# Performance work log

Hardware: AMD Instinct MI355X
Metric: run time of the kernel (lower is better)

Reference implementation:

```python
import jax, jax.numpy as jnp
import numpy as np

B, N = 4, 512
C_IN, H, W = 1024, 48, 48
IMG_H, IMG_W = 48.0, 48.0
CNN_EMB, BOX_EMB, GCN_OUT = 512, 256, 512
ROWS, COLS = 58, 30
ALPHA = 5.0
K_EDGES = 8 * N  # edges kept per image per graph

# all directed pairs (i != j) of a fully-connected graph on N nodes
_ii, _jj = np.meshgrid(np.arange(N), np.arange(N), indexing='ij')
_m = _ii != _jj
PAIRS = jnp.asarray(np.stack([_ii[_m], _jj[_m]], axis=1).astype(np.int32))  # [E,2]


def setup_inputs():
    key = jax.random.key(0)
    ks = jax.random.split(key, 12)
    x = jax.random.normal(ks[0], (B, C_IN, H, W), jnp.float32)
    # valid boxes (x1<x2, y1<y2) inside the 48x48 feature map
    p = jax.random.uniform(ks[1], (B, N, 2, 2), minval=0.0, maxval=float(W) - 2.0)
    lo = jnp.min(p, axis=2)
    hi = jnp.max(p, axis=2) + 1.0
    boxes = jnp.concatenate([lo, hi], axis=-1)  # [B,N,4] x1,y1,x2,y2

    def lin(k, fi, fo):
        return jax.random.normal(k, (fi, fo), jnp.float32) / np.sqrt(fi)

    return {
        'input': x, 'boxes': boxes,
        'im_scales': jnp.ones((B,), jnp.float32),
        'pdls': jnp.zeros((B,), jnp.float32),
        'pdts': jnp.zeros((B,), jnp.float32),
        'W_dec': jax.random.normal(ks[2], (256, C_IN, 3, 3), jnp.float32) / np.sqrt(C_IN * 9.0),
        'b_dec': jnp.zeros((256,), jnp.float32),
        'W_box': lin(ks[3], 4, BOX_EMB), 'b_box': jnp.zeros((BOX_EMB,), jnp.float32),
        'W_cnn': lin(ks[4], 256 * 4, CNN_EMB), 'b_cnn': jnp.zeros((CNN_EMB,), jnp.float32),
        'W_grow': lin(ks[5], CNN_EMB + BOX_EMB, GCN_OUT), 'b_grow': jnp.zeros((GCN_OUT,), jnp.float32),
        'W_gcol': lin(ks[6], CNN_EMB + BOX_EMB, GCN_OUT), 'b_gcol': jnp.zeros((GCN_OUT,), jnp.float32),
        'W_rcls': lin(ks[7], GCN_OUT, 2 * (ROWS - 1) * 2), 'b_rcls': jnp.zeros((2 * (ROWS - 1) * 2,), jnp.float32),
        'W_ccls': lin(ks[8], GCN_OUT, 2 * (COLS - 1) * 2), 'b_ccls': jnp.zeros((2 * (COLS - 1) * 2,), jnp.float32),
    }


def _bilinear(feat, bidx, py, px):
    # feat [B,C,H,W]; py,px [M,4] sample coords -> [M,4,C]
    Hh, Ww = feat.shape[2], feat.shape[3]
    py = jnp.clip(py, 0.0, Hh - 1.0)
    px = jnp.clip(px, 0.0, Ww - 1.0)
    y0 = jnp.floor(py).astype(jnp.int32)
    x0 = jnp.floor(px).astype(jnp.int32)
    y1 = jnp.minimum(y0 + 1, Hh - 1)
    x1 = jnp.minimum(x0 + 1, Ww - 1)
    wy = (py - y0)[..., None]
    wx = (px - x0)[..., None]
    b = bidx[:, None]
    f00 = feat[b, :, y0, x0]
    f01 = feat[b, :, y0, x1]
    f10 = feat[b, :, y1, x0]
    f11 = feat[b, :, y1, x1]
    return f00 * (1 - wy) * (1 - wx) + f01 * (1 - wy) * wx + f10 * wy * (1 - wx) + f11 * wy * wx


def _roi_align_2x2(feat, boxes, bidx):
    # roi_align output_size=2, spatial_scale=1, one sample per bin (bin center)
    x1, y1, x2, y2 = boxes[:, 0], boxes[:, 1], boxes[:, 2], boxes[:, 3]
    bw = (x2 - x1) / 2.0
    bh = (y2 - y1) / 2.0
    offs = jnp.array([0.5, 1.5], jnp.float32)
    sx = x1[:, None] + offs * bw[:, None]  # [M,2]
    sy = y1[:, None] + offs * bh[:, None]
    py = sy[:, jnp.array([0, 0, 1, 1])]  # (iy, ix) ordering
    px = sx[:, jnp.array([0, 1, 0, 1])]
    val = _bilinear(feat, bidx, py, px)  # [M,4,C]
    return jnp.transpose(val, (0, 2, 1)).reshape(val.shape[0], -1)  # [M, C*2*2]


def _edge_attrs(boxes_i, scale, pdl, pdt):
    org = (boxes_i - jnp.stack([pdl, pdt, pdl, pdt])) / scale
    cx = (org[:, 0] + org[:, 2]) * 0.5
    cy = (org[:, 1] + org[:, 3]) * 0.5
    tb_w = jnp.max(org[:, jnp.array([0, 2])])
    tb_h = jnp.max(org[:, jnp.array([1, 3])])
    s, d = PAIRS[:, 0], PAIRS[:, 1]
    row_attr = jnp.exp(-jnp.square((cy[s] - cy[d]) * ALPHA / tb_h))
    col_attr = jnp.exp(-jnp.square((cx[s] - cx[d]) * ALPHA / tb_w))
    rv, ri = jax.lax.top_k(row_attr, K_EDGES)
    cv, ci = jax.lax.top_k(col_attr, K_EDGES)
    return rv, PAIRS[ri], cv, PAIRS[ci]


def _gcn(x, Wg, bg, edges, ew, num_nodes):
    # PyG GCNConv: self-loops with weight 1, symmetric normalization
    loop = jnp.arange(num_nodes, dtype=edges.dtype)
    src = jnp.concatenate([edges[0], loop])
    dst = jnp.concatenate([edges[1], loop])
    w = jnp.concatenate([ew, jnp.ones((num_nodes,), ew.dtype)])
    deg = jax.ops.segment_sum(w, dst, num_segments=num_nodes)
    dis = jax.lax.rsqrt(deg)  # deg >= 1 thanks to self-loops
    norm = dis[src] * w * dis[dst]
    xw = x @ Wg
    agg = jax.ops.segment_sum(norm[:, None] * xw[src], dst, num_segments=num_nodes)
    return agg + bg


def _forward(input, boxes, im_scales, pdls, pdts, W_dec, b_dec, W_box, b_box,
             W_cnn, b_cnn, W_grow, b_grow, W_gcol, b_gcol, W_rcls, b_rcls, W_ccls, b_ccls):
    Bn = B * N
    flat = boxes.reshape(Bn, 4)
    # box features (relative center / size)
    cx = (flat[:, 0] + flat[:, 2]) / 2.0
    cy = (flat[:, 1] + flat[:, 3]) / 2.0
    bf = jnp.stack([cx / IMG_W, cy / IMG_H,
                    (flat[:, 2] - flat[:, 0]) / IMG_W,
                    (flat[:, 3] - flat[:, 1]) / IMG_H], axis=1)
    box_feat = jax.nn.relu(bf @ W_box + b_box)
    # decode conv + relu
    dec = jax.lax.conv_general_dilated(input, W_dec, (1, 1), 'SAME',
                                       dimension_numbers=('NCHW', 'OIHW', 'NCHW'))
    dec = jax.nn.relu(dec + b_dec[None, :, None, None])
    # roi-align 2x2 + cnn embedding
    bidx = jnp.repeat(jnp.arange(B, dtype=jnp.int32), N)
    cnn = _roi_align_2x2(dec, flat, bidx)
    cnn_feat = jax.nn.relu(cnn @ W_cnn + b_cnn)
    # per-image dense graph -> top-8N row/col edges
    rv, re, cv, ce = jax.vmap(_edge_attrs)(boxes, im_scales, pdls, pdts)
    off = (jnp.arange(B, dtype=jnp.int32) * N)[:, None, None]
    row_edge = (re + off).reshape(-1, 2).T  # [2, B*K]
    col_edge = (ce + off).reshape(-1, 2).T
    row_w = rv.reshape(-1)
    col_w = cv.reshape(-1)
    fusion = jnp.concatenate([box_feat, cnn_feat], axis=1)  # [Bn, 768]
    row_feat = jax.nn.relu(_gcn(fusion, W_grow, b_grow, row_edge, row_w, Bn))
    col_feat = jax.nn.relu(_gcn(fusion, W_gcol, b_gcol, col_edge, col_w, Bn))
    row_score = jax.nn.leaky_relu(row_feat @ W_rcls + b_rcls, 0.01).reshape(Bn, 2, ROWS - 1, 2)
    col_score = jax.nn.leaky_relu(col_feat @ W_ccls + b_ccls, 0.01).reshape(Bn, 2, COLS - 1, 2)
    return row_score, col_score


def reference(input, boxes, im_scales, pdls, pdts, W_dec, b_dec, W_box, b_box,
              W_cnn, b_cnn, W_grow, b_grow, W_gcol, b_gcol, W_rcls, b_rcls, W_ccls, b_ccls):
    return _forward(input, boxes, im_scales, pdls, pdts, W_dec, b_dec, W_box, b_box,
                    W_cnn, b_cnn, W_grow, b_grow, W_gcol, b_gcol,
                    W_rcls, b_rcls, W_ccls, b_ccls)
```

## Files before the change

kernel.cpp:

```cpp
#include <hip/hip_runtime.h>
#include <cstdint>
#include <math.h>

typedef unsigned int u32;
typedef unsigned long long u64;
typedef unsigned short ushort;

typedef __attribute__((ext_vector_type(8))) _Float16 f16x8;
typedef __attribute__((ext_vector_type(4))) _Float16 f16x4;
typedef __attribute__((ext_vector_type(4))) float f32x4;

#define NB    4
#define BnN   2048
#define NE    261632
#define NCHUNK 16
#define ECHUNK 16352
#define KEDGE 4096
#define TIECAP 2048
#define PSLICE 2359296
#define MS    64
#define TS    64

#define GLD16(gsrc, ldst)                                                    \
    __builtin_amdgcn_global_load_lds(                                        \
        (const __attribute__((address_space(1))) void*)(gsrc),               \
        (__attribute__((address_space(3))) void*)(ldst), 16, 0, 0)

__global__ __launch_bounds__(256) void cvt_x_kernel(
    const float* __restrict__ in, _Float16* __restrict__ xf)
{
    __shared__ _Float16 sh[64][49];
    int cg = blockIdx.x, y = blockIdx.y, b = blockIdx.z;
    int tid = threadIdx.x;
    for (int i = tid; i < 64 * 48; i += 256) {
        int cl = i / 48, x = i - cl * 48;
        sh[cl][x] = (_Float16)in[(((size_t)b * 1024 + cg * 64 + cl) * 48 + y) * 48 + x];
    }
    __syncthreads();
    for (int i = tid; i < 64 * 48; i += 256) {
        int x = i / 64, cl = i - x * 64;
        xf[((size_t)(b * 48 + y) * 48 + x) * 1024 + cg * 64 + cl] = sh[cl][x];
    }
}

__global__ __launch_bounds__(256) void cvt_w_kernel(
    const float* __restrict__ W, _Float16* __restrict__ wf)
{
    __shared__ _Float16 sh[9216];
    int o = blockIdx.x, tid = threadIdx.x;
    for (int g = tid; g < 9216; g += 256)
        sh[g] = (_Float16)W[(size_t)o * 9216 + g];
    __syncthreads();
    for (int g = tid; g < 9216; g += 256) {
        int tap = g >> 10, ch = g & 1023;
        wf[(size_t)o * 9216 + g] = sh[ch * 9 + tap];
    }
}

__global__ __launch_bounds__(256) void cvt_t5_kernel(
    const float* __restrict__ Wc,  _Float16* __restrict__ WcT,
    const float* __restrict__ Wgr, _Float16* __restrict__ WgrT,
    const float* __restrict__ Wgc, _Float16* __restrict__ WgcT,
    const float* __restrict__ Wr,  _Float16* __restrict__ WrT,
    const float* __restrict__ Wcc, _Float16* __restrict__ WccT)
{
    __shared__ _Float16 sh[32][33];
    int bid = blockIdx.x;
    const float* in; _Float16* out; int K, N, tx0, ty0, ntx;
    if (bid < 512)       { in = Wc;  out = WcT;  K = 1024; N = 512; ntx = 16; bid -= 0;    }
    else if (bid < 896)  { in = Wgr; out = WgrT; K = 768;  N = 512; ntx = 16; bid -= 512;  }
    else if (bid < 1280) { in = Wgc; out = WgcT; K = 768;  N = 512; ntx = 16; bid -= 896;  }
    else if (bid < 1408) { in = Wr;  out = WrT;  K = 512;  N = 228; ntx = 8;  bid -= 1280; }
    else                 { in = Wcc; out = WccT; K = 512;  N = 116; ntx = 4;  bid -= 1408; }
    tx0 = (bid % ntx) * 32;
    ty0 = (bid / ntx) * 32;
    int tx = threadIdx.x & 31, ty = threadIdx.x >> 5;
#pragma unroll
    for (int i = 0; i < 4; ++i) {
        int k = ty0 + ty + i * 8, n = tx0 + tx;
        sh[ty + i * 8][tx] = (k < K && n < N) ? (_Float16)in[(size_t)k * N + n] : (_Float16)0.f;
    }
    __syncthreads();
#pragma unroll
    for (int i = 0; i < 4; ++i) {
        int n = tx0 + ty + i * 8, k = ty0 + tx;
        if (n < N && k < K) out[(size_t)n * K + k] = sh[tx][ty + i * 8];
    }
}

#define STAGE_X(cc, BUF)                                                     \
    {                                                                        \
        _Pragma("unroll")                                                    \
        for (int it = 0; it < 8; ++it) {                                     \
            int g0 = it * 256 + wv * 64;                                     \
            if (g0 < 1920)                                                   \
                GLD16(xsrc[it] + (cc), &xS[(BUF) * 15360 + g0 * 8]);         \
        }                                                                    \
    }

#define STAGE_W(cc)                                                          \
    {                                                                        \
        _Pragma("unroll")                                                    \
        for (int it = 0; it < 5; ++it) {                                     \
            int g0 = it * 256 + wv * 64;                                     \
            if (g0 < 1152)                                                   \
                GLD16(wsrc[it] + (cc), &wS[g0 * 8]);                         \
        }                                                                    \
    }

#define LDB(BUF, R)                                                          \
    {                                                                        \
        _Pragma("unroll")                                                    \
        for (int u = 0; u < 9; ++u) {                                        \
            int nt_ = u / 3, dx_ = u % 3;                                    \
            int col = nt_ * 16 + n + dx_ - 1;                                \
            const _Float16* pa = &xb[(((R) * 4 + q) * 48 + col) * 8];        \
            if (u == 0 && n == 0)  pa = zS;                                  \
            if (u == 8 && n == 15) pa = zS;                                  \
            BUF[u] = *(const f16x8*)pa;                                      \
        }                                                                    \
    }

#define DOTAP(TAP, BLO, BHI)                                                 \
    {                                                                        \
        _Pragma("unroll")                                                    \
        for (int dx_ = 0; dx_ < 3; ++dx_) {                                  \
            f16x8 a0 = *(const f16x8*)&wS[(((TAP) + dx_) * 128 + q * 32 + n) * 8];      \
            f16x8 a1 = *(const f16x8*)&wS[(((TAP) + dx_) * 128 + q * 32 + 16 + n) * 8]; \
            _Pragma("unroll")                                                \
            for (int nt_ = 0; nt_ < 3; ++nt_) {                              \
                f16x8 blo = BLO[nt_ * 3 + dx_];                              \
                f16x8 bhi = BHI[nt_ * 3 + dx_];                              \
                acc[0][0][nt_] = __builtin_amdgcn_mfma_f32_16x16x32_f16(a0, blo, acc[0][0][nt_], 0, 0, 0); \
                acc[1][0][nt_] = __builtin_amdgcn_mfma_f32_16x16x32_f16(a1, blo, acc[1][0][nt_], 0, 0, 0); \
                acc[0][1][nt_] = __builtin_amdgcn_mfma_f32_16x16x32_f16(a0, bhi, acc[0][1][nt_], 0, 0, 0); \
                acc[1][1][nt_] = __builtin_amdgcn_mfma_f32_16x16x32_f16(a1, bhi, acc[1][1][nt_], 0, 0, 0); \
            }                                                                \
        }                                                                    \
    }
// ... 263 lines not shown
    const int lm = ln & 15, lq = ln >> 4;
    const int sr = tid >> 2, sq = tid & 3;

    const _Float16* asrc = A + (size_t)(m0 + sr) * K + sq * 8;
    const _Float16* bsrc = (n0 + sr < N) ? (Bt + (size_t)(n0 + sr) * K + sq * 8) : zbuf;

    f32x4 acc[2][2];
#pragma unroll
    for (int i = 0; i < 2; ++i)
#pragma unroll
        for (int j = 0; j < 2; ++j) acc[i][j] = (f32x4){0.f, 0.f, 0.f, 0.f};

    const int NT = K >> 5;
    GEMM_STAGE(0, 0);
#pragma unroll 1
    for (int it = 0; it < NT; ++it) {
        const int bi = it & 1;
        if (it + 1 < NT) {
            GEMM_STAGE((it + 1) * 32, bi ^ 1);
            asm volatile("s_waitcnt vmcnt(2)" ::: "memory");
        } else {
            asm volatile("s_waitcnt vmcnt(0)" ::: "memory");
        }
        __builtin_amdgcn_s_barrier();
        f16x8 af[2], bf[2];
#pragma unroll
        for (int mt = 0; mt < 2; ++mt) af[mt] = *(const f16x8*)&aS[bi][(wm * 32 + mt * 16 + lm) * 32 + lq * 8];
#pragma unroll
        for (int nt = 0; nt < 2; ++nt) bf[nt] = *(const f16x8*)&bS[bi][(wn * 32 + nt * 16 + lm) * 32 + lq * 8];
#pragma unroll
        for (int mt = 0; mt < 2; ++mt)
#pragma unroll
            for (int nt = 0; nt < 2; ++nt)
                acc[mt][nt] = __builtin_amdgcn_mfma_f32_16x16x32_f16(af[mt], bf[nt], acc[mt][nt], 0, 0, 0);
        __builtin_amdgcn_sched_barrier(0);
        __builtin_amdgcn_s_barrier();
    }

#pragma unroll
    for (int mt = 0; mt < 2; ++mt) {
#pragma unroll
        for (int nt = 0; nt < 2; ++nt) {
            int col = n0 + wn * 32 + nt * 16 + lm;
            if (col >= N) continue;
#pragma unroll
            for (int r = 0; r < 4; ++r) {
                int row = m0 + wm * 32 + mt * 16 + lq * 4 + r;
                C[(size_t)row * ldC + col] = acc[mt][nt][r];
            }
        }
    }
}

__device__ __forceinline__ float compute_sv_tb(
    const float* __restrict__ boxes, const float* __restrict__ scales,
    const float* __restrict__ pdls, const float* __restrict__ pdts,
    int b, int t, float* sv, float* red)
{
    int tid = threadIdx.x;
    float pdl = pdls[b], pdt = pdts[b], sc = scales[b];
    if (tid < 512) {
        const float* bx = boxes + (size_t)(b * 512 + tid) * 4;
        float o0 = (bx[0] - pdl) / sc;
        float o1 = (bx[1] - pdt) / sc;
        float o2 = (bx[2] - pdl) / sc;
        float o3 = (bx[3] - pdt) / sc;
        sv[tid]  = (t == 0) ? (o1 + o3) * 0.5f : (o0 + o2) * 0.5f;
        red[tid] = (t == 0) ? fmaxf(o1, o3)    : fmaxf(o0, o2);
    }
    __syncthreads();
    for (int s = 256; s > 0; s >>= 1) {
        if (tid < s) red[tid] = fmaxf(red[tid], red[tid + s]);
        __syncthreads();
    }
    float tbv = red[0];
    __syncthreads();
    return tbv;
}

#define QBITS(e, QB)                                                   \
    {                                                                  \
        int i_ = (e) / 511; int jj_ = (e) - i_ * 511;                  \
        int j_ = jj_ + (jj_ >= i_ ? 1 : 0);                            \
        float diff_ = sv[i_] - sv[j_];                                 \
        float u_ = (diff_ * 5.0f) / tbv;                               \
        float q_ = u_ * u_;                                            \
        QB = __float_as_uint(q_);                                      \
    }

__global__ __launch_bounds__(1024) void histA_kernel(
    const float* __restrict__ boxes, const float* __restrict__ scales,
    const float* __restrict__ pdls, const float* __restrict__ pdts,
    u32* __restrict__ gpart)
{
    __shared__ float sv[512]; __shared__ float red[512];
    __shared__ u32 lh[4096];
    const int sel = blockIdx.y, b = sel >> 1, t = sel & 1;
    const int tid = threadIdx.x;
    for (int i = tid; i < 4096; i += 1024) lh[i] = 0;
    const float tbv = compute_sv_tb(boxes, scales, pdls, pdts, b, t, sv, red);
    const int e1 = min((int)(blockIdx.x + 1) * ECHUNK, NE);
    for (int e = blockIdx.x * ECHUNK + tid; e < e1; e += 1024) {
        u32 qb; QBITS(e, qb);
        atomicAdd(&lh[qb >> 20], 1u);
    }
    __syncthreads();
    u32* G = gpart + ((size_t)sel * NCHUNK + blockIdx.x) * 4096;
    for (int i = tid; i < 4096; i += 1024) G[i] = lh[i];
}

__global__ __launch_bounds__(1024) void scanA_kernel(
    const u32* __restrict__ gpart, u32* __restrict__ meta)
{
    const int sel = blockIdx.x, tid = threadIdx.x;
    __shared__ u32 bins[4096];
    __shared__ u32 sc[2][1024];
    for (int b = tid; b < 4096; b += 1024) {
        u32 s = 0;
        for (int c = 0; c < NCHUNK; ++c) s += gpart[((size_t)sel * NCHUNK + c) * 4096 + b];
        bins[b] = s;
    }
    __syncthreads();
    u32 part = 0;
#pragma unroll
    for (int j = 0; j < 4; ++j) part += bins[tid * 4 + j];
    sc[0][tid] = part;
    __syncthreads();
    int src = 0;
    for (int st = 1; st < 1024; st <<= 1) {
        sc[1 - src][tid] = sc[src][tid] + (tid >= st ? sc[src][tid - st] : 0);
        __syncthreads(); src = 1 - src;
    }
    u32 inc = sc[src][tid], exc = inc - part;
    if (exc < (u32)KEDGE && (u32)KEDGE <= inc) {
        u32 cum = exc;
        for (int j = 0; j < 4; ++j) {
            u32 c = bins[tid * 4 + j];
            if (cum + c >= (u32)KEDGE) {
                meta[sel * MS + 0] = (u32)(tid * 4 + j);
                meta[sel * MS + 1] = (u32)KEDGE - cum;
                break;
            }
            cum += c;
        }
    }
}

__global__ __launch_bounds__(1024) void histB_kernel(
    const float* __restrict__ boxes, const float* __restrict__ scales,
    const float* __restrict__ pdls, const float* __restrict__ pdts,
    const u32* __restrict__ meta, u32* __restrict__ gpart)
{
    __shared__ float sv[512]; __shared__ float red[512];
    __shared__ u32 lh[4096];
    const int sel = blockIdx.y, b = sel >> 1, t = sel & 1;
    const int tid = threadIdx.x;
    for (int i = tid; i < 4096; i += 1024) lh[i] = 0;
    const float tbv = compute_sv_tb(boxes, scales, pdls, pdts, b, t, sv, red);
    const u32 p12 = meta[sel * MS + 0];
    const int e1 = min((int)(blockIdx.x + 1) * ECHUNK, NE);
    for (int e = blockIdx.x * ECHUNK + tid; e < e1; e += 1024) {
        u32 qb; QBITS(e, qb);
        if ((qb >> 20) == p12) atomicAdd(&lh[(qb >> 8) & 0xFFF], 1u);
    }
    __syncthreads();
    u32* G = gpart + ((size_t)sel * NCHUNK + blockIdx.x) * 4096;
    for (int i = tid; i < 4096; i += 1024) G[i] = lh[i];
}

__global__ __launch_bounds__(1024) void scanB_kernel(
    const u32* __restrict__ gpart, u32* __restrict__ meta)
{
    const int sel = blockIdx.x, tid = threadIdx.x;
    const u32 TH = meta[sel * MS + 1];
    __shared__ u32 bins[4096];
    __shared__ u32 sc[2][1024];
    for (int b = tid; b < 4096; b += 1024) {
        u32 s = 0;
        for (int c = 0; c < NCHUNK; ++c) s += gpart[((size_t)sel * NCHUNK + c) * 4096 + b];
        bins[b] = s;
    }
    __syncthreads();
    u32 part = 0;
#pragma unroll
    for (int j = 0; j < 4; ++j) part += bins[tid * 4 + j];
    sc[0][tid] = part;
    __syncthreads();
    int src = 0;
    for (int st = 1; st < 1024; st <<= 1) {
        sc[1 - src][tid] = sc[src][tid] + (tid >= st ? sc[src][tid - st] : 0);
        __syncthreads(); src = 1 - src;
    }
    u32 inc = sc[src][tid], exc = inc - part;
    if (exc < TH && TH <= inc) {
        u32 cum = exc;
        for (int j = 0; j < 4; ++j) {
            u32 c = bins[tid * 4 + j];
            if (cum + c >= TH) {
                meta[sel * MS + 6] = (meta[sel * MS + 0] << 12) | (u32)(tid * 4 + j);
                meta[sel * MS + 7] = TH - cum;
                break;
            }
            cum += c;
        }
    }
}

__global__ __launch_bounds__(1024) void histC_kernel(
    const float* __restrict__ boxes, const float* __restrict__ scales,
    const float* __restrict__ pdls, const float* __restrict__ pdts,
    const u32* __restrict__ meta, u32* __restrict__ gpart)
{
    __shared__ float sv[512]; __shared__ float red[512];
    __shared__ u32 lh[256];
    const int sel = blockIdx.y, b = sel >> 1, t = sel & 1;
    const int tid = threadIdx.x;
    if (tid < 256) lh[tid] = 0;
    const float tbv = compute_sv_tb(boxes, scales, pdls, pdts, b, t, sv, red);
    const u32 p24 = meta[sel * MS + 6];
    const int e1 = min((int)(blockIdx.x + 1) * ECHUNK, NE);
    for (int e = blockIdx.x * ECHUNK + tid; e < e1; e += 1024) {
        u32 qb; QBITS(e, qb);
        if ((qb >> 8) == p24) atomicAdd(&lh[qb & 0xFF], 1u);
    }
    __syncthreads();
    u32* G = gpart + ((size_t)sel * NCHUNK + blockIdx.x) * 256;
    if (tid < 256) G[tid] = lh[tid];
}

__global__ __launch_bounds__(256) void scanC_kernel(
    const u32* __restrict__ gpart, u32* __restrict__ meta)
{
    const int sel = blockIdx.x, tid = threadIdx.x;
    const u32 TH = meta[sel * MS + 7];
    __shared__ u32 bins[256];
    __shared__ u32 sc[2][256];
    __shared__ u32 s_qstar;
    u32 s = 0;
    for (int c = 0; c < NCHUNK; ++c) s += gpart[((size_t)sel * NCHUNK + c) * 256 + tid];
    bins[tid] = s;
    sc[0][tid] = s;
    __syncthreads();
    int src = 0;
    for (int st = 1; st < 256; st <<= 1) {
        sc[1 - src][tid] = sc[src][tid] + (tid >= st ? sc[src][tid - st] : 0);
        __syncthreads(); src = 1 - src;
    }
    u32 inc = sc[src][tid], exc = inc - bins[tid];
    if (exc < TH && TH <= inc)
        s_qstar = (meta[sel * MS + 6] << 8) | (u32)tid;
    __syncthreads();
    if (tid == 0) {
        u32 prefix = s_qstar;
        float qstar = __uint_as_float(prefix);
        float wstar = (float)exp(-(double)qstar);
        u32 lo = 0, hi = prefix;
        while (lo < hi) {
            u32 mid = (lo + hi) >> 1;
            float wm = (float)exp(-(double)__uint_as_float(mid));
            if (wm > wstar) lo = mid + 1; else hi = mid;
        }
        meta[sel * MS + 2] = lo;
        lo = prefix; hi = 0x7F800000u;
        while (lo < hi) {
            u32 mid = (lo + hi + 1) >> 1;
            float wm = (float)exp(-(double)__uint_as_float(mid));
            if (wm < wstar) hi = mid - 1; else lo = mid;
        }
        meta[sel * MS + 3] = lo;
        meta[sel * MS + 4] = __float_as_uint(wstar);
    }
}

__global__ __launch_bounds__(1024) void emit_kernel(
    const float* __restrict__ boxes, const float* __restrict__ scales,
    const float* __restrict__ pdls, const float* __restrict__ pdts,
    u32* __restrict__ meta, int* __restrict__ tiebuf, int* __restrict__ tiecnt,
    int* __restrict__ es, int* __restrict__ ed, float* __restrict__ ewt,
    int* __restrict__ indeg, float* __restrict__ degw)
{
    __shared__ float sv[512]; __shared__ float red[512];
    __shared__ int s_wcnt, s_tcnt, s_wbase, s_tbase;
    const int sel = blockIdx.y, b = sel >> 1, t = sel & 1;
    const int tid = threadIdx.x;
    const float tbv = compute_sv_tb(boxes, scales, pdls, pdts, b, t, sv, red);
    const u32 qlo = meta[sel * MS + 2], qhi = meta[sel * MS + 3];
    const int base = t * 16384 + b * 4096;
    const int e0 = blockIdx.x * ECHUNK + tid;
    const int e1 = min((int)(blockIdx.x + 1) * ECHUNK, NE);
    if (tid == 0) { s_wcnt = 0; s_tcnt = 0; }
    __syncthreads();
    int myw = 0, myt = 0;
    for (int e = e0; e < e1; e += 1024) {
        u32 qb; QBITS(e, qb);
        if (qb < qlo) ++myw;
        else if (qb <= qhi) ++myt;
    }
    if (myw) atomicAdd(&s_wcnt, myw);
    if (myt) atomicAdd(&s_tcnt, myt);
    __syncthreads();
    if (tid == 0) {
        s_wbase = (s_wcnt > 0) ? (int)atomicAdd(&meta[sel * MS + 5], (u32)s_wcnt) : 0;
        s_tbase = (s_tcnt > 0) ? atomicAdd(&tiecnt[sel * TS], s_tcnt) : 0;
        s_wcnt = 0; s_tcnt = 0;
    }
    __syncthreads();
    for (int e = e0; e < e1; e += 1024) {
        u32 qb; QBITS(e, qb);
        if (qb < qlo) {
            int i = e / 511; int jj = e - i * 511; int j = jj + (jj >= i ? 1 : 0);
            float wval = (float)exp(-(double)__uint_as_float(qb));
            int slot = s_wbase + atomicAdd(&s_wcnt, 1);
            es[base + slot] = b * 512 + i;
            ed[base + slot] = b * 512 + j;
            ewt[base + slot] = wval;
            atomicAdd(&indeg[t * 2048 + b * 512 + j], 1);
            atomicAdd(&degw[t * 2048 + b * 512 + j], wval);
        } else if (qb <= qhi) {
            int p = s_tbase + atomicAdd(&s_tcnt, 1);
            if (p < TIECAP) tiebuf[sel * TIECAP + p] = e;
        }
    }
}

__global__ __launch_bounds__(1024) void tie_scan_fill_kernel(
    u32* __restrict__ meta, const int* __restrict__ tiebuf, const int* __restrict__ tiecnt,
    int* __restrict__ es, int* __restrict__ ed, float* __restrict__ ewt,
    int* __restrict__ indeg, float* __restrict__ degw,
    int* __restrict__ offs, float* __restrict__ dis, int* __restrict__ csr)
{
    __shared__ int bufA[2048], bufB[2048];
    __shared__ int fill_l[2048];
    const int t = blockIdx.x, tid = threadIdx.x;
    for (int b = 0; b < 4; ++b) {
        int sel = b * 2 + t;
        int m = min(tiecnt[sel * TS], TIECAP);
        int r = KEDGE - (int)meta[sel * MS + 5];
        float wt = __uint_as_float(meta[sel * MS + 4]);
        int base = t * 16384 + b * 4096;
        for (int k = tid; k < m; k += 1024) {
            int e = tiebuf[sel * TIECAP + k];
            int rank = 0;
            for (int l = 0; l < m; ++l) rank += (tiebuf[sel * TIECAP + l] < e) ? 1 : 0;
            if (rank < r) {
                int i = e / 511; int jj = e - i * 511; int j = jj + (jj >= i ? 1 : 0);
                int slot = (int)atomicAdd(&meta[sel * MS + 5], 1u);
                es[base + slot] = b * 512 + i;
                ed[base + slot] = b * 512 + j;
                ewt[base + slot] = wt;
                atomicAdd(&indeg[t * 2048 + b * 512 + j], 1);
                atomicAdd(&degw[t * 2048 + b * 512 + j], wt);
            }
        }
    }
    __threadfence();
    __syncthreads();
    bufA[tid] = indeg[t * 2048 + tid];
    bufA[tid + 1024] = indeg[t * 2048 + tid + 1024];
    fill_l[tid] = 0; fill_l[tid + 1024] = 0;
    __syncthreads();
    int* src = bufA; int* dst = bufB;
    for (int st = 1; st < 2048; st <<= 1) {
        dst[tid] = src[tid] + (tid >= st ? src[tid - st] : 0);
        int k1 = tid + 1024;
        dst[k1] = src[k1] + (k1 >= st ? src[k1 - st] : 0);
        __syncthreads();
        int* tmp = src; src = dst; dst = tmp;
    }
    int off0 = (tid == 0) ? 0 : src[tid - 1];
    int off1 = src[tid + 1023];
    __syncthreads();
    dst[tid] = off0; dst[tid + 1024] = off1;
    offs[t * 2048 + tid] = off0;
    offs[t * 2048 + tid + 1024] = off1;
// ... 38 lines not shown
}

extern "C" void kernel_launch(void* const* d_in, const int* in_sizes, int n_in,
                              void* d_out, int out_size, void* d_ws, size_t ws_size,
                              hipStream_t stream)
{
    const float* x      = (const float*)d_in[0];
    const float* boxes  = (const float*)d_in[1];
    const float* scales = (const float*)d_in[2];
    const float* pdls   = (const float*)d_in[3];
    const float* pdts   = (const float*)d_in[4];
    const float* W_dec  = (const float*)d_in[5];
    const float* b_dec  = (const float*)d_in[6];
    const float* W_box  = (const float*)d_in[7];
    const float* b_box  = (const float*)d_in[8];
    const float* W_cnn  = (const float*)d_in[9];
    const float* b_cnn  = (const float*)d_in[10];
    const float* W_grow = (const float*)d_in[11];
    const float* b_grow = (const float*)d_in[12];
    const float* W_gcol = (const float*)d_in[13];
    const float* b_gcol = (const float*)d_in[14];
    const float* W_rcls = (const float*)d_in[15];
    const float* b_rcls = (const float*)d_in[16];
    const float* W_ccls = (const float*)d_in[17];
    const float* b_ccls = (const float*)d_in[18];

    char* ws = (char*)d_ws;
    size_t off = 0;
    auto alloc = [&](size_t bytes) -> void* {
        void* p = ws + off;
        off = (off + bytes + 255) & ~(size_t)255;
        return p;
    };
    _Float16* xf16   = (_Float16*)alloc((size_t)4 * 2304 * 1024 * 2);
    _Float16* wf16   = (_Float16*)alloc((size_t)256 * 9216 * 2);
    _Float16* dec    = (_Float16*)alloc((size_t)4 * 2304 * 256 * 2);
    float*    pbuf   = (float*)   alloc((size_t)4 * PSLICE * 4);
    _Float16* cnn    = (_Float16*)alloc((size_t)2048 * 1024 * 2);
    _Float16* fusion = (_Float16*)alloc((size_t)2048 * 768 * 2);
    _Float16* WcT    = (_Float16*)alloc((size_t)512 * 1024 * 2);
    _Float16* WgrT   = (_Float16*)alloc((size_t)512 * 768 * 2);
    _Float16* WgcT   = (_Float16*)alloc((size_t)512 * 768 * 2);
    _Float16* WrT    = (_Float16*)alloc((size_t)228 * 512 * 2);
    _Float16* WccT   = (_Float16*)alloc((size_t)116 * 512 * 2);
    float* xw        = (float*)alloc((size_t)2097152 * 4);
    _Float16* feats  = (_Float16*)alloc((size_t)2 * 2048 * 512 * 2);
    int*  es     = (int*)  alloc((size_t)2 * 16384 * 4);
    int*  ed     = (int*)  alloc((size_t)2 * 16384 * 4);
    float* ewt   = (float*)alloc((size_t)2 * 16384 * 4);
    int*  offsA  = (int*)  alloc((size_t)4096 * 4);
    float* dis   = (float*)alloc((size_t)4096 * 4);
    int*  csr    = (int*)  alloc((size_t)2 * 16384 * 4);
    int*  tiebuf = (int*)  alloc((size_t)8 * TIECAP * 4);
    u32*  gpartA = (u32*)  alloc((size_t)8 * NCHUNK * 4096 * 4);
    u32*  gpartB = (u32*)  alloc((size_t)8 * NCHUNK * 4096 * 4);
    u32*  gpartC = (u32*)  alloc((size_t)8 * NCHUNK * 256 * 4);
    size_t z0 = off;
    u32*  meta   = (u32*)  alloc((size_t)8 * MS * 4);
    int*  tiecnt = (int*)  alloc((size_t)8 * TS * 4);
    int*  indeg  = (int*)  alloc((size_t)4096 * 4);
    float* degw  = (float*)alloc((size_t)4096 * 4);
    _Float16* zbuf = (_Float16*)alloc((size_t)4096);
    size_t z1 = off;

    float* out = (float*)d_out;

    hipMemsetAsync(ws + z0, 0, z1 - z0, stream);

    cvt_x_kernel<<<dim3(16, 48, 4), 256, 0, stream>>>(x, xf16);
    cvt_w_kernel<<<256, 256, 0, stream>>>(W_dec, wf16);
    conv_part_kernel<<<dim3(768), 256, 0, stream>>>(xf16, wf16, zbuf, pbuf);
    conv_sum_kernel<<<2304, 256, 0, stream>>>(pbuf, b_dec, dec);
    roi_box_kernel<<<2048, 256, 0, stream>>>(dec, boxes, W_box, b_box, cnn, fusion);
    cvt_t5_kernel<<<1472, 256, 0, stream>>>(W_cnn, WcT, W_grow, WgrT, W_gcol, WgcT,
                                            W_rcls, WrT, W_ccls, WccT);
    gemm16_kernel<1, _Float16><<<dim3(8, 32), 256, 0, stream>>>(cnn, WcT, zbuf, b_cnn, fusion + 256, 2048, 512, 1024, 768);
    histA_kernel<<<dim3(NCHUNK, 8), 1024, 0, stream>>>(boxes, scales, pdls, pdts, gpartA);
    scanA_kernel<<<8, 1024, 0, stream>>>(gpartA, meta);
    histB_kernel<<<dim3(NCHUNK, 8), 1024, 0, stream>>>(boxes, scales, pdls, pdts, meta, gpartB);
    scanB_kernel<<<8, 1024, 0, stream>>>(gpartB, meta);
    histC_kernel<<<dim3(NCHUNK, 8), 1024, 0, stream>>>(boxes, scales, pdls, pdts, meta, gpartC);
    scanC_kernel<<<8, 256, 0, stream>>>(gpartC, meta);
    emit_kernel<<<dim3(NCHUNK, 8), 1024, 0, stream>>>(boxes, scales, pdls, pdts, meta,
                                                      tiebuf, tiecnt, es, ed, ewt, indeg, degw);
    tie_scan_fill_kernel<<<2, 1024, 0, stream>>>(meta, tiebuf, tiecnt, es, ed, ewt,
                                                 indeg, degw, offsA, dis, csr);
    gemm16z_kernel<<<dim3(8, 32, 2), 256, 0, stream>>>(fusion, WgrT, WgcT, zbuf, xw, xw + 1048576,
                                                       2048, 512, 768, 512);
    gcn_agg_kernel<<<dim3(2048, 2), 256, 0, stream>>>(xw, xw + 1048576, b_grow, b_gcol,
                                                      es, ewt, csr, offsA, indeg, dis,
                                                      feats, feats + (size_t)2048 * 512);
    gemm16_kernel<2, float><<<dim3(4, 32), 256, 0, stream>>>(feats, WrT, zbuf, b_rcls, out, 2048, 228, 512, 228);
    gemm16_kernel<2, float><<<dim3(2, 32), 256, 0, stream>>>(feats + (size_t)2048 * 512, WccT, zbuf, b_ccls,
                                                             out + (size_t)2048 * 228, 2048, 116, 512, 116);
}
```

Measured before the change: 353.3 us.

## Merge launches: fused prep, single-block edge selection, batched head GEMMs

```diff
diff --git a/kernel.cpp b/kernel.cpp
--- a/kernel.cpp
+++ b/kernel.cpp
@@ -13,8 +13,6 @@
 #define NB    4
 #define BnN   2048
 #define NE    261632
-#define NCHUNK 16
-#define ECHUNK 16352
 #define KEDGE 4096
 #define TIECAP 2048
 #define PSLICE 2359296
@@ -26,65 +24,63 @@
         (const __attribute__((address_space(1))) void*)(gsrc),               \
         (__attribute__((address_space(3))) void*)(ldst), 16, 0, 0)
 
-__global__ __launch_bounds__(256) void cvt_x_kernel(
-    const float* __restrict__ in, _Float16* __restrict__ xf)
-{
-    __shared__ _Float16 sh[64][49];
-    int cg = blockIdx.x, y = blockIdx.y, b = blockIdx.z;
-    int tid = threadIdx.x;
-    for (int i = tid; i < 64 * 48; i += 256) {
-        int cl = i / 48, x = i - cl * 48;
-        sh[cl][x] = (_Float16)in[(((size_t)b * 1024 + cg * 64 + cl) * 48 + y) * 48 + x];
-    }
-    __syncthreads();
-    for (int i = tid; i < 64 * 48; i += 256) {
-        int x = i / 64, cl = i - x * 64;
-        xf[((size_t)(b * 48 + y) * 48 + x) * 1024 + cg * 64 + cl] = sh[cl][x];
-    }
-}
-
-__global__ __launch_bounds__(256) void cvt_w_kernel(
-    const float* __restrict__ W, _Float16* __restrict__ wf)
-{
-    __shared__ _Float16 sh[9216];
-    int o = blockIdx.x, tid = threadIdx.x;
-    for (int g = tid; g < 9216; g += 256)
-        sh[g] = (_Float16)W[(size_t)o * 9216 + g];
-    __syncthreads();
-    for (int g = tid; g < 9216; g += 256) {
-        int tap = g >> 10, ch = g & 1023;
-        wf[(size_t)o * 9216 + g] = sh[ch * 9 + tap];
-    }
-}
-
-__global__ __launch_bounds__(256) void cvt_t5_kernel(
+__global__ __launch_bounds__(256) void prep_kernel(
+    const float* __restrict__ in, _Float16* __restrict__ xf,
+    const float* __restrict__ W, _Float16* __restrict__ wf,
     const float* __restrict__ Wc,  _Float16* __restrict__ WcT,
     const float* __restrict__ Wgr, _Float16* __restrict__ WgrT,
     const float* __restrict__ Wgc, _Float16* __restrict__ WgcT,
     const float* __restrict__ Wr,  _Float16* __restrict__ WrT,
     const float* __restrict__ Wcc, _Float16* __restrict__ WccT)
 {
-    __shared__ _Float16 sh[32][33];
-    int bid = blockIdx.x;
-    const float* in; _Float16* out; int K, N, tx0, ty0, ntx;
-    if (bid < 512)       { in = Wc;  out = WcT;  K = 1024; N = 512; ntx = 16; bid -= 0;    }
-    else if (bid < 896)  { in = Wgr; out = WgrT; K = 768;  N = 512; ntx = 16; bid -= 512;  }
-    else if (bid < 1280) { in = Wgc; out = WgcT; K = 768;  N = 512; ntx = 16; bid -= 896;  }
-    else if (bid < 1408) { in = Wr;  out = WrT;  K = 512;  N = 228; ntx = 8;  bid -= 1280; }
-    else                 { in = Wcc; out = WccT; K = 512;  N = 116; ntx = 4;  bid -= 1408; }
-    tx0 = (bid % ntx) * 32;
-    ty0 = (bid / ntx) * 32;
-    int tx = threadIdx.x & 31, ty = threadIdx.x >> 5;
-#pragma unroll
-    for (int i = 0; i < 4; ++i) {
-        int k = ty0 + ty + i * 8, n = tx0 + tx;
-        sh[ty + i * 8][tx] = (k < K && n < N) ? (_Float16)in[(size_t)k * N + n] : (_Float16)0.f;
-    }
-    __syncthreads();
-#pragma unroll
-    for (int i = 0; i < 4; ++i) {
-        int n = tx0 + ty + i * 8, k = ty0 + tx;
-        if (n < N && k < K) out[(size_t)n * K + k] = sh[tx][ty + i * 8];
+    __shared__ _Float16 sh[9216];
+    const int bid = blockIdx.x;
+    const int tid = threadIdx.x;
+    if (bid < 3072) {
+        _Float16 (*shx)[49] = (_Float16(*)[49])sh;
+        int cg = bid & 15, rem = bid >> 4;
+        int y = rem % 48, b = rem / 48;
+        for (int i = tid; i < 64 * 48; i += 256) {
+            int cl = i / 48, x = i - cl * 48;
+            shx[cl][x] = (_Float16)in[(((size_t)b * 1024 + cg * 64 + cl) * 48 + y) * 48 + x];
+        }
+        __syncthreads();
+        for (int i = tid; i < 64 * 48; i += 256) {
+            int x = i / 64, cl = i - x * 64;
+            xf[((size_t)(b * 48 + y) * 48 + x) * 1024 + cg * 64 + cl] = shx[cl][x];
+        }
+    } else if (bid < 3328) {
+        int o = bid - 3072;
+        for (int g = tid; g < 9216; g += 256)
+            sh[g] = (_Float16)W[(size_t)o * 9216 + g];
+        __syncthreads();
+        for (int g = tid; g < 9216; g += 256) {
+            int tap = g >> 10, ch = g & 1023;
+            wf[(size_t)o * 9216 + g] = sh[ch * 9 + tap];
+        }
+    } else {
+        _Float16 (*sht)[33] = (_Float16(*)[33])sh;
+        int b2 = bid - 3328;
+        const float* inm; _Float16* outm; int K, N, tx0, ty0, ntx;
+        if (b2 < 512)       { inm = Wc;  outm = WcT;  K = 1024; N = 512; ntx = 16; b2 -= 0;    }
+        else if (b2 < 896)  { inm = Wgr; outm = WgrT; K = 768;  N = 512; ntx = 16; b2 -= 512;  }
+        else if (b2 < 1280) { inm = Wgc; outm = WgcT; K = 768;  N = 512; ntx = 16; b2 -= 896;  }
+        else if (b2 < 1408) { inm = Wr;  outm = WrT;  K = 512;  N = 228; ntx = 8;  b2 -= 1280; }
+        else                { inm = Wcc; outm = WccT; K = 512;  N = 116; ntx = 4;  b2 -= 1408; }
+        tx0 = (b2 % ntx) * 32;
+        ty0 = (b2 / ntx) * 32;
+        int tx = tid & 31, ty = tid >> 5;
+#pragma unroll
+        for (int i = 0; i < 4; ++i) {
+            int k = ty0 + ty + i * 8, n = tx0 + tx;
+            sht[ty + i * 8][tx] = (k < K && n < N) ? (_Float16)inm[(size_t)k * N + n] : (_Float16)0.f;
+        }
+        __syncthreads();
+#pragma unroll
+        for (int i = 0; i < 4; ++i) {
+            int n = tx0 + ty + i * 8, k = ty0 + tx;
+            if (n < N && k < K) outm[(size_t)n * K + k] = sht[tx][ty + i * 8];
+        }
     }
 }
 
@@ -454,6 +450,84 @@
     }
 }
 
+__global__ __launch_bounds__(256) void gemm16h_kernel(
+    const _Float16* __restrict__ A0, const _Float16* __restrict__ A1,
+    const _Float16* __restrict__ Bt0, const _Float16* __restrict__ Bt1,
+    const _Float16* __restrict__ zbuf,
+    const float* __restrict__ bias0, const float* __restrict__ bias1,
+    float* __restrict__ C0, float* __restrict__ C1,
+    int M, int N0, int N1, int K)
+{
+    const int z = blockIdx.z;
+    const _Float16* __restrict__ A  = z ? A1 : A0;
+    const _Float16* __restrict__ Bt = z ? Bt1 : Bt0;
+    const float* __restrict__ bias  = z ? bias1 : bias0;
+    float* __restrict__ C           = z ? C1 : C0;
+    const int N = z ? N1 : N0;
+    const int ldC = N;
+    const int n0 = blockIdx.x * 64, m0 = blockIdx.y * 64;
+    if (n0 >= N) return;
+    __shared__ _Float16 aS[2][256 * 8];
+    __shared__ _Float16 bS[2][256 * 8];
+    const int tid = threadIdx.x;
+    const int wv = tid >> 6, ln = tid & 63;
+    const int wm = wv & 1, wn = wv >> 1;
+    const int lm = ln & 15, lq = ln >> 4;
+    const int sr = tid >> 2, sq = tid & 3;
+
+    const _Float16* asrc = A + (size_t)(m0 + sr) * K + sq * 8;
+    const _Float16* bsrc = (n0 + sr < N) ? (Bt + (size_t)(n0 + sr) * K + sq * 8) : zbuf;
+
+    f32x4 acc[2][2];
+#pragma unroll
+    for (int i = 0; i < 2; ++i)
+#pragma unroll
+        for (int j = 0; j < 2; ++j) acc[i][j] = (f32x4){0.f, 0.f, 0.f, 0.f};
+
+    const int NT = K >> 5;
+    GEMM_STAGE(0, 0);
+#pragma unroll 1
+    for (int it = 0; it < NT; ++it) {
+        const int bi = it & 1;
+        if (it + 1 < NT) {
+            GEMM_STAGE((it + 1) * 32, bi ^ 1);
+            asm volatile("s_waitcnt vmcnt(2)" ::: "memory");
+        } else {
+            asm volatile("s_waitcnt vmcnt(0)" ::: "memory");
+        }
+        __builtin_amdgcn_s_barrier();
+        f16x8 af[2], bf[2];
+#pragma unroll
+        for (int mt = 0; mt < 2; ++mt) af[mt] = *(const f16x8*)&aS[bi][(wm * 32 + mt * 16 + lm) * 32 + lq * 8];
+#pragma unroll
+        for (int nt = 0; nt < 2; ++nt) bf[nt] = *(const f16x8*)&bS[bi][(wn * 32 + nt * 16 + lm) * 32 + lq * 8];
+#pragma unroll
+        for (int mt = 0; mt < 2; ++mt)
+#pragma unroll
+            for (int nt = 0; nt < 2; ++nt)
+                acc[mt][nt] = __builtin_amdgcn_mfma_f32_16x16x32_f16(af[mt], bf[nt], acc[mt][nt], 0, 0, 0);
+        __builtin_amdgcn_sched_barrier(0);
+        __builtin_amdgcn_s_barrier();
+    }
+
+#pragma unroll
+    for (int mt = 0; mt < 2; ++mt) {
+#pragma unroll
+        for (int nt = 0; nt < 2; ++nt) {
+            int col = n0 + wn * 32 + nt * 16 + lm;
+            if (col >= N) continue;
+            float bs = bias[col];
+#pragma unroll
+            for (int r = 0; r < 4; ++r) {
+                int row = m0 + wm * 32 + mt * 16 + lq * 4 + r;
+                float v = acc[mt][nt][r] + bs;
+                v = (v >= 0.f) ? v : 0.01f * v;
+                C[(size_t)row * ldC + col] = v;
+            }
+        }
+    }
+}
+
 __device__ __forceinline__ float compute_sv_tb(
     const float* __restrict__ boxes, const float* __restrict__ scales,
     const float* __restrict__ pdls, const float* __restrict__ pdts,
@@ -490,167 +564,108 @@
         QB = __float_as_uint(q_);                                      \
     }
 
-__global__ __launch_bounds__(1024) void histA_kernel(
+__global__ __launch_bounds__(1024) void edge_mega_kernel(
     const float* __restrict__ boxes, const float* __restrict__ scales,
     const float* __restrict__ pdls, const float* __restrict__ pdts,
-    u32* __restrict__ gpart)
+    u32* __restrict__ meta, int* __restrict__ tiebuf, int* __restrict__ tiecnt,
+    int* __restrict__ es, int* __restrict__ ed, float* __restrict__ ewt,
+    int* __restrict__ indeg, float* __restrict__ degw)
 {
     __shared__ float sv[512]; __shared__ float red[512];
     __shared__ u32 lh[4096];
-    const int sel = blockIdx.y, b = sel >> 1, t = sel & 1;
+    __shared__ u32 sc[2][1024];
+    __shared__ u32 s_p12, s_need1, s_p24, s_need2, s_qstar;
+    __shared__ u32 s_qlo, s_qhi, s_wstar;
+    __shared__ int s_w, s_t;
+    const int sel = blockIdx.x, b = sel >> 1, t = sel & 1;
     const int tid = threadIdx.x;
+    const float tbv = compute_sv_tb(boxes, scales, pdls, pdts, b, t, sv, red);
+
     for (int i = tid; i < 4096; i += 1024) lh[i] = 0;
-    const float tbv = compute_sv_tb(boxes, scales, pdls, pdts, b, t, sv, red);
-    const int e1 = min((int)(blockIdx.x + 1) * ECHUNK, NE);
-    for (int e = blockIdx.x * ECHUNK + tid; e < e1; e += 1024) {
+    __syncthreads();
+    for (int e = tid; e < NE; e += 1024) {
         u32 qb; QBITS(e, qb);
         atomicAdd(&lh[qb >> 20], 1u);
     }
     __syncthreads();
-    u32* G = gpart + ((size_t)sel * NCHUNK + blockIdx.x) * 4096;
-    for (int i = tid; i < 4096; i += 1024) G[i] = lh[i];
-}
-
-__global__ __launch_bounds__(1024) void scanA_kernel(
-    const u32* __restrict__ gpart, u32* __restrict__ meta)
-{
-    const int sel = blockIdx.x, tid = threadIdx.x;
-    __shared__ u32 bins[4096];
-    __shared__ u32 sc[2][1024];
-    for (int b = tid; b < 4096; b += 1024) {
-        u32 s = 0;
-        for (int c = 0; c < NCHUNK; ++c) s += gpart[((size_t)sel * NCHUNK + c) * 4096 + b];
-        bins[b] = s;
-    }
-    __syncthreads();
-    u32 part = 0;
-#pragma unroll
-    for (int j = 0; j < 4; ++j) part += bins[tid * 4 + j];
-    sc[0][tid] = part;
-    __syncthreads();
-    int src = 0;
-    for (int st = 1; st < 1024; st <<= 1) {
-        sc[1 - src][tid] = sc[src][tid] + (tid >= st ? sc[src][tid - st] : 0);
-        __syncthreads(); src = 1 - src;
-    }
-    u32 inc = sc[src][tid], exc = inc - part;
-    if (exc < (u32)KEDGE && (u32)KEDGE <= inc) {
-        u32 cum = exc;
-        for (int j = 0; j < 4; ++j) {
-            u32 c = bins[tid * 4 + j];
-            if (cum + c >= (u32)KEDGE) {
-                meta[sel * MS + 0] = (u32)(tid * 4 + j);
-                meta[sel * MS + 1] = (u32)KEDGE - cum;
-                break;
+    {
+        u32 part = 0;
+#pragma unroll
+        for (int j = 0; j < 4; ++j) part += lh[tid * 4 + j];
+        sc[0][tid] = part;
+        __syncthreads();
+        int src = 0;
+        for (int st = 1; st < 1024; st <<= 1) {
+            sc[1 - src][tid] = sc[src][tid] + (tid >= st ? sc[src][tid - st] : 0);
+            __syncthreads(); src = 1 - src;
+        }
+        u32 inc = sc[src][tid], exc = inc - part;
+        if (exc < (u32)KEDGE && (u32)KEDGE <= inc) {
+            u32 cum = exc;
+            for (int j = 0; j < 4; ++j) {
+                u32 c = lh[tid * 4 + j];
+                if (cum + c >= (u32)KEDGE) { s_p12 = (u32)(tid * 4 + j); s_need1 = (u32)KEDGE - cum; break; }
+                cum += c;
             }
-            cum += c;
-        }
-    }
-}
-
-__global__ __launch_bounds__(1024) void histB_kernel(
-    const float* __restrict__ boxes, const float* __restrict__ scales,
-    const float* __restrict__ pdls, const float* __restrict__ pdts,
-    const u32* __restrict__ meta, u32* __restrict__ gpart)
-{
-    __shared__ float sv[512]; __shared__ float red[512];
-    __shared__ u32 lh[4096];
-    const int sel = blockIdx.y, b = sel >> 1, t = sel & 1;
-    const int tid = threadIdx.x;
+        }
+    }
+    __syncthreads();
+    const u32 p12 = s_p12, need1 = s_need1;
+
+    __syncthreads();
     for (int i = tid; i < 4096; i += 1024) lh[i] = 0;
-    const float tbv = compute_sv_tb(boxes, scales, pdls, pdts, b, t, sv, red);
-    const u32 p12 = meta[sel * MS + 0];
-    const int e1 = min((int)(blockIdx.x + 1) * ECHUNK, NE);
-    for (int e = blockIdx.x * ECHUNK + tid; e < e1; e += 1024) {
+    __syncthreads();
+    for (int e = tid; e < NE; e += 1024) {
         u32 qb; QBITS(e, qb);
         if ((qb >> 20) == p12) atomicAdd(&lh[(qb >> 8) & 0xFFF], 1u);
     }
     __syncthreads();
-    u32* G = gpart + ((size_t)sel * NCHUNK + blockIdx.x) * 4096;
-    for (int i = tid; i < 4096; i += 1024) G[i] = lh[i];
-}
-
-__global__ __launch_bounds__(1024) void scanB_kernel(
-    const u32* __restrict__ gpart, u32* __restrict__ meta)
-{
-    const int sel = blockIdx.x, tid = threadIdx.x;
-    const u32 TH = meta[sel * MS + 1];
-    __shared__ u32 bins[4096];
-    __shared__ u32 sc[2][1024];
-    for (int b = tid; b < 4096; b += 1024) {
-        u32 s = 0;
-        for (int c = 0; c < NCHUNK; ++c) s += gpart[((size_t)sel * NCHUNK + c) * 4096 + b];
-        bins[b] = s;
-    }
-    __syncthreads();
-    u32 part = 0;
-#pragma unroll
-    for (int j = 0; j < 4; ++j) part += bins[tid * 4 + j];
-    sc[0][tid] = part;
-    __syncthreads();
-    int src = 0;
-    for (int st = 1; st < 1024; st <<= 1) {
-        sc[1 - src][tid] = sc[src][tid] + (tid >= st ? sc[src][tid - st] : 0);
-        __syncthreads(); src = 1 - src;
-    }
-    u32 inc = sc[src][tid], exc = inc - part;
-    if (exc < TH && TH <= inc) {
-        u32 cum = exc;
-        for (int j = 0; j < 4; ++j) {
-            u32 c = bins[tid * 4 + j];
-            if (cum + c >= TH) {
-                meta[sel * MS + 6] = (meta[sel * MS + 0] << 12) | (u32)(tid * 4 + j);
-                meta[sel * MS + 7] = TH - cum;
-                break;
+    {
+        u32 part = 0;
+#pragma unroll
+        for (int j = 0; j < 4; ++j) part += lh[tid * 4 + j];
+        sc[0][tid] = part;
+        __syncthreads();
+        int src = 0;
+        for (int st = 1; st < 1024; st <<= 1) {
+            sc[1 - src][tid] = sc[src][tid] + (tid >= st ? sc[src][tid - st] : 0);
+            __syncthreads(); src = 1 - src;
+        }
+        u32 inc = sc[src][tid], exc = inc - part;
+        if (exc < need1 && need1 <= inc) {
+            u32 cum = exc;
+            for (int j = 0; j < 4; ++j) {
+                u32 c = lh[tid * 4 + j];
+                if (cum + c >= need1) { s_p24 = (p12 << 12) | (u32)(tid * 4 + j); s_need2 = need1 - cum; break; }
+                cum += c;
             }
-            cum += c;
-        }
-    }
-}
-
-__global__ __launch_bounds__(1024) void histC_kernel(
-    const float* __restrict__ boxes, const float* __restrict__ scales,
-    const float* __restrict__ pdls, const float* __restrict__ pdts,
-    const u32* __restrict__ meta, u32* __restrict__ gpart)
-{
-    __shared__ float sv[512]; __shared__ float red[512];
-    __shared__ u32 lh[256];
-    const int sel = blockIdx.y, b = sel >> 1, t = sel & 1;
-    const int tid = threadIdx.x;
+        }
+    }
+    __syncthreads();
+    const u32 p24 = s_p24, need2 = s_need2;
+
+    __syncthreads();
     if (tid < 256) lh[tid] = 0;
-    const float tbv = compute_sv_tb(boxes, scales, pdls, pdts, b, t, sv, red);
-    const u32 p24 = meta[sel * MS + 6];
-    const int e1 = min((int)(blockIdx.x + 1) * ECHUNK, NE);
-    for (int e = blockIdx.x * ECHUNK + tid; e < e1; e += 1024) {
+    __syncthreads();
+    for (int e = tid; e < NE; e += 1024) {
         u32 qb; QBITS(e, qb);
         if ((qb >> 8) == p24) atomicAdd(&lh[qb & 0xFF], 1u);
     }
     __syncthreads();
-    u32* G = gpart + ((size_t)sel * NCHUNK + blockIdx.x) * 256;
-    if (tid < 256) G[tid] = lh[tid];
-}
-
-__global__ __launch_bounds__(256) void scanC_kernel(
-    const u32* __restrict__ gpart, u32* __restrict__ meta)
-{
-    const int sel = blockIdx.x, tid = threadIdx.x;
-    const u32 TH = meta[sel * MS + 7];
-    __shared__ u32 bins[256];
-    __shared__ u32 sc[2][256];
-    __shared__ u32 s_qstar;
-    u32 s = 0;
-    for (int c = 0; c < NCHUNK; ++c) s += gpart[((size_t)sel * NCHUNK + c) * 256 + tid];
-    bins[tid] = s;
-    sc[0][tid] = s;
-    __syncthreads();
-    int src = 0;
-    for (int st = 1; st < 256; st <<= 1) {
-        sc[1 - src][tid] = sc[src][tid] + (tid >= st ? sc[src][tid - st] : 0);
-        __syncthreads(); src = 1 - src;
-    }
-    u32 inc = sc[src][tid], exc = inc - bins[tid];
-    if (exc < TH && TH <= inc)
-        s_qstar = (meta[sel * MS + 6] << 8) | (u32)tid;
+    {
+        if (tid < 256) sc[0][tid] = lh[tid];
+        __syncthreads();
+        int src = 0;
+        for (int st = 1; st < 256; st <<= 1) {
+            if (tid < 256)
+                sc[1 - src][tid] = sc[src][tid] + (tid >= st ? sc[src][tid - st] : 0);
+            __syncthreads(); src = 1 - src;
+        }
+        if (tid < 256) {
+            u32 inc = sc[src][tid], exc = inc - lh[tid];
+            if (exc < need2 && need2 <= inc) s_qstar = (p24 << 8) | (u32)tid;
+        }
+    }
     __syncthreads();
     if (tid == 0) {
         u32 prefix = s_qstar;
@@ -662,66 +677,42 @@
             float wm = (float)exp(-(double)__uint_as_float(mid));
             if (wm > wstar) lo = mid + 1; else hi = mid;
         }
-        meta[sel * MS + 2] = lo;
+        s_qlo = lo;
         lo = prefix; hi = 0x7F800000u;
         while (lo < hi) {
             u32 mid = (lo + hi + 1) >> 1;
             float wm = (float)exp(-(double)__uint_as_float(mid));
             if (wm < wstar) hi = mid - 1; else lo = mid;
         }
-        meta[sel * MS + 3] = lo;
-        meta[sel * MS + 4] = __float_as_uint(wstar);
-    }
-}
-
-__global__ __launch_bounds__(1024) void emit_kernel(
-    const float* __restrict__ boxes, const float* __restrict__ scales,
-    const float* __restrict__ pdls, const float* __restrict__ pdts,
-    u32* __restrict__ meta, int* __restrict__ tiebuf, int* __restrict__ tiecnt,
-    int* __restrict__ es, int* __restrict__ ed, float* __restrict__ ewt,
-    int* __restrict__ indeg, float* __restrict__ degw)
-{
-    __shared__ float sv[512]; __shared__ float red[512];
-    __shared__ int s_wcnt, s_tcnt, s_wbase, s_tbase;
-    const int sel = blockIdx.y, b = sel >> 1, t = sel & 1;
-    const int tid = threadIdx.x;
-    const float tbv = compute_sv_tb(boxes, scales, pdls, pdts, b, t, sv, red);
-    const u32 qlo = meta[sel * MS + 2], qhi = meta[sel * MS + 3];
+        s_qhi = lo;
+        s_wstar = __float_as_uint(wstar);
+        meta[sel * MS + 4] = s_wstar;
+        s_w = 0; s_t = 0;
+    }
+    __syncthreads();
+    const u32 qlo = s_qlo, qhi = s_qhi;
     const int base = t * 16384 + b * 4096;
-    const int e0 = blockIdx.x * ECHUNK + tid;
-    const int e1 = min((int)(blockIdx.x + 1) * ECHUNK, NE);
-    if (tid == 0) { s_wcnt = 0; s_tcnt = 0; }
-    __syncthreads();
-    int myw = 0, myt = 0;
-    for (int e = e0; e < e1; e += 1024) {
-        u32 qb; QBITS(e, qb);
-        if (qb < qlo) ++myw;
-        else if (qb <= qhi) ++myt;
-    }
-    if (myw) atomicAdd(&s_wcnt, myw);
-    if (myt) atomicAdd(&s_tcnt, myt);
-    __syncthreads();
-    if (tid == 0) {
-        s_wbase = (s_wcnt > 0) ? (int)atomicAdd(&meta[sel * MS + 5], (u32)s_wcnt) : 0;
-        s_tbase = (s_tcnt > 0) ? atomicAdd(&tiecnt[sel * TS], s_tcnt) : 0;
-        s_wcnt = 0; s_tcnt = 0;
-    }
-    __syncthreads();
-    for (int e = e0; e < e1; e += 1024) {
+
+    for (int e = tid; e < NE; e += 1024) {
         u32 qb; QBITS(e, qb);
         if (qb < qlo) {
             int i = e / 511; int jj = e - i * 511; int j = jj + (jj >= i ? 1 : 0);
             float wval = (float)exp(-(double)__uint_as_float(qb));
-            int slot = s_wbase + atomicAdd(&s_wcnt, 1);
+            int slot = atomicAdd(&s_w, 1);
             es[base + slot] = b * 512 + i;
             ed[base + slot] = b * 512 + j;
             ewt[base + slot] = wval;
             atomicAdd(&indeg[t * 2048 + b * 512 + j], 1);
             atomicAdd(&degw[t * 2048 + b * 512 + j], wval);
         } else if (qb <= qhi) {
-            int p = s_tbase + atomicAdd(&s_tcnt, 1);
-            if (p < TIECAP) tiebuf[sel * TIECAP + p] = e;
-        }
+            int ppos = atomicAdd(&s_t, 1);
+            if (ppos < TIECAP) tiebuf[sel * TIECAP + ppos] = e;
+        }
+    }
+    __syncthreads();
+    if (tid == 0) {
+        meta[sel * MS + 5] = (u32)s_w;
+        tiecnt[sel * TS] = s_t;
     }
 }
 
@@ -866,9 +857,6 @@
     float* dis   = (float*)alloc((size_t)4096 * 4);
     int*  csr    = (int*)  alloc((size_t)2 * 16384 * 4);
     int*  tiebuf = (int*)  alloc((size_t)8 * TIECAP * 4);
-    u32*  gpartA = (u32*)  alloc((size_t)8 * NCHUNK * 4096 * 4);
-    u32*  gpartB = (u32*)  alloc((size_t)8 * NCHUNK * 4096 * 4);
-    u32*  gpartC = (u32*)  alloc((size_t)8 * NCHUNK * 256 * 4);
     size_t z0 = off;
     u32*  meta   = (u32*)  alloc((size_t)8 * MS * 4);
     int*  tiecnt = (int*)  alloc((size_t)8 * TS * 4);
@@ -881,22 +869,15 @@
 
     hipMemsetAsync(ws + z0, 0, z1 - z0, stream);
 
-    cvt_x_kernel<<<dim3(16, 48, 4), 256, 0, stream>>>(x, xf16);
-    cvt_w_kernel<<<256, 256, 0, stream>>>(W_dec, wf16);
+    prep_kernel<<<4800, 256, 0, stream>>>(x, xf16, W_dec, wf16,
+                                          W_cnn, WcT, W_grow, WgrT, W_gcol, WgcT,
+                                          W_rcls, WrT, W_ccls, WccT);
     conv_part_kernel<<<dim3(768), 256, 0, stream>>>(xf16, wf16, zbuf, pbuf);
     conv_sum_kernel<<<2304, 256, 0, stream>>>(pbuf, b_dec, dec);
     roi_box_kernel<<<2048, 256, 0, stream>>>(dec, boxes, W_box, b_box, cnn, fusion);
-    cvt_t5_kernel<<<1472, 256, 0, stream>>>(W_cnn, WcT, W_grow, WgrT, W_gcol, WgcT,
-                                            W_rcls, WrT, W_ccls, WccT);
     gemm16_kernel<1, _Float16><<<dim3(8, 32), 256, 0, stream>>>(cnn, WcT, zbuf, b_cnn, fusion + 256, 2048, 512, 1024, 768);
-    histA_kernel<<<dim3(NCHUNK, 8), 1024, 0, stream>>>(boxes, scales, pdls, pdts, gpartA);
-    scanA_kernel<<<8, 1024, 0, stream>>>(gpartA, meta);
-    histB_kernel<<<dim3(NCHUNK, 8), 1024, 0, stream>>>(boxes, scales, pdls, pdts, meta, gpartB);
-    scanB_kernel<<<8, 1024, 0, stream>>>(gpartB, meta);
-    histC_kernel<<<dim3(NCHUNK, 8), 1024, 0, stream>>>(boxes, scales, pdls, pdts, meta, gpartC);
-    scanC_kernel<<<8, 256, 0, stream>>>(gpartC, meta);
-    emit_kernel<<<dim3(NCHUNK, 8), 1024, 0, stream>>>(boxes, scales, pdls, pdts, meta,
-                                                      tiebuf, tiecnt, es, ed, ewt, indeg, degw);
+    edge_mega_kernel<<<8, 1024, 0, stream>>>(boxes, scales, pdls, pdts, meta,
+                                             tiebuf, tiecnt, es, ed, ewt, indeg, degw);
     tie_scan_fill_kernel<<<2, 1024, 0, stream>>>(meta, tiebuf, tiecnt, es, ed, ewt,
                                                  indeg, degw, offsA, dis, csr);
     gemm16z_kernel<<<dim3(8, 32, 2), 256, 0, stream>>>(fusion, WgrT, WgcT, zbuf, xw, xw + 1048576,
@@ -904,7 +885,8 @@
     gcn_agg_kernel<<<dim3(2048, 2), 256, 0, stream>>>(xw, xw + 1048576, b_grow, b_gcol,
                                                       es, ewt, csr, offsA, indeg, dis,
                                                       feats, feats + (size_t)2048 * 512);
-    gemm16_kernel<2, float><<<dim3(4, 32), 256, 0, stream>>>(feats, WrT, zbuf, b_rcls, out, 2048, 228, 512, 228);
-    gemm16_kernel<2, float><<<dim3(2, 32), 256, 0, stream>>>(feats + (size_t)2048 * 512, WccT, zbuf, b_ccls,
-                                                             out + (size_t)2048 * 228, 2048, 116, 512, 116);
-}
+    gemm16h_kernel<<<dim3(4, 32, 2), 256, 0, stream>>>(feats, feats + (size_t)2048 * 512,
+                                                       WrT, WccT, zbuf, b_rcls, b_ccls,
+                                                       out, out + (size_t)2048 * 228,
+                                                       2048, 228, 116, 512);
+}
```

Measured after the change: 572.4 us. +62.0%, slower.
